# Kernel tuning notes

Measured on AMD Instinct MI355X. Metric: run time of the kernel, lower is better.

## Reference

```python
import jax, jax.numpy as jnp
import numpy as np

L = 9  # local window size


def local_windows(x, l):
    # x: (n, c, h, w) -> (n, c, l*l, h, w): all l*l shifted views (zero-padded),
    # equivalent to F.unfold(x, kernel=(l,l), stride=1, padding=l//2).
    n, c, h, w = x.shape
    pad = l // 2
    xp = jnp.pad(x, ((0, 0), (0, 0), (pad, pad), (pad, pad)))
    views = [xp[:, :, i:i + h, j:j + w] for i in range(l) for j in range(l)]
    return jnp.stack(views, axis=2)


def setup_inputs() -> dict:
    key = jax.random.key(0)
    k1, k2, k3 = jax.random.split(key, 3)
    n, c, h, w = 2, 128, 64, 64
    ft = jax.random.normal(k1, (n, c, h, w), dtype=jnp.float32)
    fk = jax.random.normal(k2, (n, c, h, w), dtype=jnp.float32)
    # 1x1 conv weight shared between key and query projections: (out_c, in_c)
    W = jax.random.normal(k3, (128, 128), dtype=jnp.float32) * (1.0 / np.sqrt(128))
    return {"ft": ft, "fk": fk, "W": W}


def reference(ft, fk, W):
    # 1x1 conv == channel matmul
    key = jnp.einsum('oi,nihw->nohw', W, ft)    # key from frame t
    query = jnp.einsum('oi,nihw->nohw', W, fk)  # query from frame k
    # f_similar(query, key, L): per-pixel query dotted with L*L local keys
    key_win = local_windows(key, L)             # (n, c, L*L, h, w)
    sim = jnp.einsum('nchw,nckhw->nhwk', query, key_win)  # (n, h, w, L*L)
    weight = jax.nn.softmax(sim, axis=-1)
    # f_weighting(ft, weight, L): weighted sum of L*L local raw-ft vectors
    ft_win = local_windows(ft, L)                # (n, c, L*L, h, w)
    out = jnp.einsum('nckhw,nhwk->nchw', ft_win, weight)
    return out
```

## Files before the change

kernel.cpp:

```cpp
#include <hip/hip_runtime.h>
#include <hip/hip_bf16.h>


#define Hh 64
#define Ww 64
#define Cc 128
#define Nn 2
#define KK 81
#define HW (Hh * Ww)
#define CHW (Cc * HW)
#define P_TOT (Nn * HW)

typedef _Float16 h8 __attribute__((ext_vector_type(8)));
typedef _Float16 h4 __attribute__((ext_vector_type(4)));
typedef float f4v __attribute__((ext_vector_type(4)));

#ifndef __has_builtin
#define __has_builtin(x) 0
#endif

#if __has_builtin(__builtin_amdgcn_ds_read_tr16_b64_v4f16)
#define TR_BUILTIN 1
typedef __fp16 g4 __attribute__((__vector_size__(4 * sizeof(__fp16))));
static __device__ __forceinline__ h4 tr16(const _Float16* p) {
    g4 r = __builtin_amdgcn_ds_read_tr16_b64_v4f16(
        (__attribute__((address_space(3))) g4*)p);
    return __builtin_bit_cast(h4, r);
}
#else
#define TR_BUILTIN 0
static __device__ __forceinline__ h4 tr16(const _Float16* p) {
    h4 r;
    asm volatile("ds_read_b64_tr_b16 %0, %1"
                 : "=v"(r)
                 : "v"((__attribute__((address_space(3))) _Float16*)p));
    return r;
}
#endif

__global__ __launch_bounds__(256) void proj_kernel(const float* __restrict__ ft,
                                                   const float* __restrict__ fk,
                                                   const float* __restrict__ Wm,
                                                   _Float16* __restrict__ Qbuf,
                                                   _Float16* __restrict__ Kbuf,
                                                   _Float16* __restrict__ fth) {
    __shared__ __align__(16) _Float16 Wth[128 * 136];
    __shared__ __align__(16) _Float16 xkh[16 * 136];
    __shared__ __align__(16) _Float16 xqh[16 * 136];
    const int t = threadIdx.x;
    const int p0 = blockIdx.x * 16;
    const int nn = p0 >> 12;
    const int gbase = nn * CHW + (p0 & 4095);

#pragma unroll 4
    for (int e = t; e < 4096; e += 256) {
        const int n = e >> 5, ch = e & 31;
        const float4 v = *(const float4*)&Wm[n * 128 + (ch << 2)];
        h4 hv; hv[0] = (_Float16)v.x; hv[1] = (_Float16)v.y;
               hv[2] = (_Float16)v.z; hv[3] = (_Float16)v.w;
        *(h4*)&Wth[n * 136 + (ch << 2)] = hv;
    }
#pragma unroll
    for (int e = t; e < 512; e += 256) {
        const int c = e >> 2, pc = e & 3;
        const float4 vk = *(const float4*)&ft[gbase + c * HW + (pc << 2)];
        const float4 vq = *(const float4*)&fk[gbase + c * HW + (pc << 2)];
        const int px = pc << 2;
        xkh[(px    ) * 136 + c] = (_Float16)vk.x;
        xkh[(px + 1) * 136 + c] = (_Float16)vk.y;
        xkh[(px + 2) * 136 + c] = (_Float16)vk.z;
        xkh[(px + 3) * 136 + c] = (_Float16)vk.w;
        xqh[(px    ) * 136 + c] = (_Float16)vq.x;
        xqh[(px + 1) * 136 + c] = (_Float16)vq.y;
        xqh[(px + 2) * 136 + c] = (_Float16)vq.z;
        xqh[(px + 3) * 136 + c] = (_Float16)vq.w;
    }
    __syncthreads();

    {
        const int px = t >> 4, cq = t & 15;
        *(h8*)&fth[(size_t)(p0 + px) * 128 + (cq << 3)] =
            *(const h8*)&xkh[px * 136 + (cq << 3)];
    }

    const int lane = t & 63, wv = t >> 6;
    const int quad = lane >> 4, l15 = lane & 15;
    const _Float16* xs = (wv >> 1) ? xqh : xkh;
    _Float16* dst = (wv >> 1) ? Qbuf : Kbuf;
    const int nt0 = (wv & 1) << 2;
    const int abase = l15 * 136 + (quad << 3);
    const h8 a0 = *(const h8*)&xs[abase];
    const h8 a1 = *(const h8*)&xs[abase + 32];
    const h8 a2 = *(const h8*)&xs[abase + 64];
    const h8 a3 = *(const h8*)&xs[abase + 96];
#pragma unroll
    for (int ni = 0; ni < 4; ++ni) {
        const int nt = nt0 + ni;
        const int bbase = (nt * 16 + l15) * 136 + (quad << 3);
        const h8 b0 = *(const h8*)&Wth[bbase];
        const h8 b1 = *(const h8*)&Wth[bbase + 32];
        const h8 b2 = *(const h8*)&Wth[bbase + 64];
        const h8 b3 = *(const h8*)&Wth[bbase + 96];
        f4v acc = {0.f, 0.f, 0.f, 0.f};
        acc = __builtin_amdgcn_mfma_f32_16x16x32_f16(a0, b0, acc, 0, 0, 0);
        acc = __builtin_amdgcn_mfma_f32_16x16x32_f16(a1, b1, acc, 0, 0, 0);
        acc = __builtin_amdgcn_mfma_f32_16x16x32_f16(a2, b2, acc, 0, 0, 0);
        acc = __builtin_amdgcn_mfma_f32_16x16x32_f16(a3, b3, acc, 0, 0, 0);
        const int col = nt * 16 + l15;
        const size_t rb = (size_t)(p0 + (quad << 2)) * 128 + col;
#pragma unroll
        for (int r = 0; r < 4; ++r)
            dst[rb + (size_t)r * 128] = (_Float16)acc[r];
    }
}

#define FTL_CH 2312
__global__ __launch_bounds__(256, 4) void sim_weight_kernel(const _Float16* __restrict__ Qbuf,
                                                            const _Float16* __restrict__ Kbuf,
                                                            const _Float16* __restrict__ fth,
                                                            float* __restrict__ out) {
    __shared__ __align__(16) unsigned char smem[40720];
    _Float16* Ksw  = (_Float16*)smem;
    _Float16* Qsw  = (_Float16*)(smem + 36864);
    _Float16* ftl  = (_Float16*)smem;
    _Float16* simb = (_Float16*)(smem + 39168);
    float*    redM = (float*)(smem + 40464);
    float*    redS = (float*)(smem + 40592);

    const int t  = threadIdx.x;
    const int b  = blockIdx.x;
    const int x0 = (b & 7) << 3;
    const int y  = (b >> 3) & 63;
    const int nn = b >> 9;
    const int pg0 = (nn << 12) + (y << 6) + x0;

#pragma unroll 3
    for (int e = t; e < 144 * 16; e += 256) {
        const int v = e >> 4, ci = e & 15;
        const int gx = x0 + (v & 15) - 4;
        const int gy = y + (v >> 4) - 4;
        h8 val = {0, 0, 0, 0, 0, 0, 0, 0};
        if ((unsigned)gx < 64u && (unsigned)gy < 64u)
            val = *(const h8*)&Kbuf[(size_t)((nn << 12) + (gy << 6) + gx) * 128 + (ci << 3)];
        *(h8*)&Ksw[(v << 7) + ((ci ^ (v & 15)) << 3)] = val;
    }
    if (t < 128) {
        const int v = t >> 4, ci = t & 15;
        *(h8*)&Qsw[(v << 7) + ((ci ^ v) << 3)] =
            *(const h8*)&Qbuf[(size_t)(pg0 + v) * 128 + (ci << 3)];
    }
    __syncthreads();

    h8 pf[9];
#pragma unroll
    for (int i = 0; i < 9; ++i) {
        const int e = t + (i << 8);
        const int v = e >> 4, ci = e & 15;
        const int gx = x0 + (v & 15) - 4;
        const int gy = y + (v >> 4) - 4;
        h8 val = {0, 0, 0, 0, 0, 0, 0, 0};
        if ((unsigned)gx < 64u && (unsigned)gy < 64u)
            val = *(const h8*)&fth[(size_t)((nn << 12) + (gy << 6) + gx) * 128 + (ci << 3)];
        pf[i] = val;
    }

    const int lane = t & 63, wv = t >> 6;
    const int quad = lane >> 4, l15 = lane & 15;
    const int qrow = l15 & 7;
    h8 qb[4];
#pragma unroll
    for (int kc = 0; kc < 4; ++kc) {
        const int ci = (kc << 2) + quad;
        qb[kc] = *(const h8*)&Qsw[(qrow << 7) + ((ci ^ qrow) << 3)];
    }
    const int r0 = wv, r1 = wv + 4;
    f4v acc0 = {0.f,0.f,0.f,0.f}, acc1 = acc0, acc2 = acc0;
#pragma unroll
    for (int kc = 0; kc < 4; ++kc) {
        const int ci = (kc << 2) + quad;
        const h8 kA = *(const h8*)&Ksw[(((r0 << 4) + l15) << 7) + ((ci ^ l15) << 3)];
        const h8 kB = *(const h8*)&Ksw[(((r1 << 4) + l15) << 7) + ((ci ^ l15) << 3)];
        const h8 kC = *(const h8*)&Ksw[(((8  << 4) + l15) << 7) + ((ci ^ l15) << 3)];
        acc0 = __builtin_amdgcn_mfma_f32_16x16x32_f16(kA, qb[kc], acc0, 0, 0, 0);
        acc1 = __builtin_amdgcn_mfma_f32_16x16x32_f16(kB, qb[kc], acc1, 0, 0, 0);
        acc2 = __builtin_amdgcn_mfma_f32_16x16x32_f16(kC, qb[kc], acc2, 0, 0, 0);
    }

    float m = -3.0e38f;
#pragma unroll
    for (int reg = 0; reg < 4; ++reg) {
        const int dx = (quad << 2) + reg - l15;
        const bool ok = (l15 < 8) && ((unsigned)dx < 9u);
        if (ok) {
            m = fmaxf(m, fmaxf(acc0[reg], acc1[reg]));
            m = fmaxf(m, acc2[reg]);
        }
    }
    m = fmaxf(m, __shfl_xor(m, 16));
    m = fmaxf(m, __shfl_xor(m, 32));
    if (quad == 0 && l15 < 8) redM[(wv << 3) + l15] = m;
    __syncthreads();

#pragma unroll
    for (int i = 0; i < 9; ++i) {
        const int e = t + (i << 8);
        const int v = e >> 4, ci = e & 15;
        *(h8*)&ftl[(ci >> 1) * FTL_CH + (v << 4) + ((ci & 1) << 3)] = pf[i];
    }

    const float mm = fmaxf(fmaxf(redM[qrow], redM[8 + qrow]),
                           fmaxf(redM[16 + qrow], redM[24 + qrow]));
    float ssum = 0.f;
#pragma unroll
    for (int reg = 0; reg < 4; ++reg) {
        const int dx = (quad << 2) + reg - l15;
        const bool ok = (l15 < 8) && ((unsigned)dx < 9u);
        const float e0 = ok ? __expf(acc0[reg] - mm) : 0.f;
        const float e1 = ok ? __expf(acc1[reg] - mm) : 0.f;
        const float e2 = (ok && wv == 0) ? __expf(acc2[reg] - mm) : 0.f;
        if (ok)            simb[((r0 * 9 + dx) << 3) + l15] = (_Float16)e0;
        if (ok)            simb[((r1 * 9 + dx) << 3) + l15] = (_Float16)e1;
        if (ok && wv == 0) simb[((8  * 9 + dx) << 3) + l15] = (_Float16)e2;
        ssum += e0 + e1 + e2;
    }
    ssum += __shfl_xor(ssum, 16);
    ssum += __shfl_xor(ssum, 32);
    if (quad == 0 && l15 < 8) redS[(wv << 3) + l15] = ssum;
    __syncthreads();

    const _Float16* ftc0 = ftl + wv * FTL_CH;
    const _Float16* ftc1 = ftl + (wv + 4) * FTL_CH;
    h4 bfr[18];
#pragma unroll
    for (int r = 0; r < 9; ++r) {
        bfr[r]     = tr16(ftc0 + (r << 8) + (lane << 2));
        bfr[9 + r] = tr16(ftc1 + (r << 8) + (lane << 2));
    }

#if !TR_BUILTIN
    asm volatile("s_waitcnt lgkmcnt(0)");
    __builtin_amdgcn_sched_barrier(0);
#endif

    f4v aw0 = {0.f, 0.f, 0.f, 0.f}, aw1 = aw0;
#pragma unroll
    for (int r = 0; r < 9; ++r) {
        h4 afr;
#pragma unroll
        for (int j = 0; j < 4; ++j) {
            const int dx = (quad << 2) + j - qrow;
            const bool ok = (unsigned)dx < 9u;
            afr[j] = ok ? simb[(((r * 9 + dx) << 3) + qrow)] : (_Float16)0.f;
        }
        aw0 = __builtin_amdgcn_mfma_f32_16x16x16f16(afr, bfr[r],     aw0, 0, 0, 0);
        aw1 = __builtin_amdgcn_mfma_f32_16x16x16f16(afr, bfr[9 + r], aw1, 0, 0, 0);
    }

    if (quad < 2) {
        const int q4 = quad << 2;
        const float4 rs0 = *(const float4*)&redS[q4];
        const float4 rs1 = *(const float4*)&redS[8 + q4];
        const float4 rs2 = *(const float4*)&redS[16 + q4];
        const float4 rs3 = *(const float4*)&redS[24 + q4];
        const float iv0 = 1.f / (rs0.x + rs1.x + rs2.x + rs3.x);
        const float iv1 = 1.f / (rs0.y + rs1.y + rs2.y + rs3.y);
        const float iv2 = 1.f / (rs0.z + rs1.z + rs2.z + rs3.z);
        const float iv3 = 1.f / (rs0.w + rs1.w + rs2.w + rs3.w);
        const int xb = (y << 6) + x0 + q4;
        const size_t ob0 = ((size_t)((nn << 7) + (wv << 4) + l15) << 12) + xb;
        const size_t ob1 = ((size_t)((nn << 7) + ((wv + 4) << 4) + l15) << 12) + xb;
        float4 o0, o1;
        o0.x = aw0[0] * iv0; o0.y = aw0[1] * iv1; o0.z = aw0[2] * iv2; o0.w = aw0[3] * iv3;
        o1.x = aw1[0] * iv0; o1.y = aw1[1] * iv1; o1.z = aw1[2] * iv2; o1.w = aw1[3] * iv3;
        *(float4*)&out[ob0] = o0;
        *(float4*)&out[ob1] = o1;
    }
}

extern "C" void kernel_launch(void* const* d_in, const int* in_sizes, int n_in,
                              void* d_out, int out_size, void* d_ws, size_t ws_size,
                              hipStream_t stream) {
    const float* ft = (const float*)d_in[0];
    const float* fk = (const float*)d_in[1];
    const float* Wm = (const float*)d_in[2];
    float* out = (float*)d_out;

    _Float16* wsh  = (_Float16*)d_ws;
    _Float16* Qbuf = wsh;
    _Float16* Kbuf = wsh + 1048576;
    _Float16* fth  = wsh + 2097152;

    proj_kernel<<<512, 256, 0, stream>>>(ft, fk, Wm, Qbuf, Kbuf, fth);
    sim_weight_kernel<<<1024, 256, 0, stream>>>(Qbuf, Kbuf, fth, out);
}
```

Measured before the change: 76.79 us.

## Fuse projection into similarity kernel, recomputing key projection per window tile

Merges the 1x1-conv projection kernel and the similarity/weighting kernel into a single kernel. Each block loads the raw fp32 ft halo window (9x16 pixels) and its 8 query pixels from fk, converts them to fp16 in shared memory, and runs the key and query projections with MFMA before the existing softmax and weighting stages. The raw ft tile then serves directly as the weighting operand. This removes the intermediate Q/K/fth global buffers and one launch, at the cost of recomputing the key projection for overlapping halos (about 18x redundant work), reloading W in every block, and doubling shared memory, which lowers occupancy to 2 blocks per CU.

```diff
diff --git a/kernel.cpp b/kernel.cpp
--- a/kernel.cpp
+++ b/kernel.cpp
@@ -9,7 +9,8 @@
 #define KK 81
 #define HW (Hh * Ww)
 #define CHW (Cc * HW)
-#define P_TOT (Nn * HW)
+
+#define FTL_CH 2312
 
 typedef _Float16 h8 __attribute__((ext_vector_type(8)));
 typedef _Float16 h4 __attribute__((ext_vector_type(4)));
@@ -38,135 +39,114 @@
 }
 #endif
 
-__global__ __launch_bounds__(256) void proj_kernel(const float* __restrict__ ft,
-                                                   const float* __restrict__ fk,
-                                                   const float* __restrict__ Wm,
-                                                   _Float16* __restrict__ Qbuf,
-                                                   _Float16* __restrict__ Kbuf,
-                                                   _Float16* __restrict__ fth) {
-    __shared__ __align__(16) _Float16 Wth[128 * 136];
-    __shared__ __align__(16) _Float16 xkh[16 * 136];
-    __shared__ __align__(16) _Float16 xqh[16 * 136];
-    const int t = threadIdx.x;
-    const int p0 = blockIdx.x * 16;
-    const int nn = p0 >> 12;
-    const int gbase = nn * CHW + (p0 & 4095);
-
-#pragma unroll 4
-    for (int e = t; e < 4096; e += 256) {
-        const int n = e >> 5, ch = e & 31;
-        const float4 v = *(const float4*)&Wm[n * 128 + (ch << 2)];
-        h4 hv; hv[0] = (_Float16)v.x; hv[1] = (_Float16)v.y;
-               hv[2] = (_Float16)v.z; hv[3] = (_Float16)v.w;
-        *(h4*)&Wth[n * 136 + (ch << 2)] = hv;
-    }
-#pragma unroll
-    for (int e = t; e < 512; e += 256) {
-        const int c = e >> 2, pc = e & 3;
-        const float4 vk = *(const float4*)&ft[gbase + c * HW + (pc << 2)];
-        const float4 vq = *(const float4*)&fk[gbase + c * HW + (pc << 2)];
-        const int px = pc << 2;
-        xkh[(px    ) * 136 + c] = (_Float16)vk.x;
-        xkh[(px + 1) * 136 + c] = (_Float16)vk.y;
-        xkh[(px + 2) * 136 + c] = (_Float16)vk.z;
-        xkh[(px + 3) * 136 + c] = (_Float16)vk.w;
-        xqh[(px    ) * 136 + c] = (_Float16)vq.x;
-        xqh[(px + 1) * 136 + c] = (_Float16)vq.y;
-        xqh[(px + 2) * 136 + c] = (_Float16)vq.z;
-        xqh[(px + 3) * 136 + c] = (_Float16)vq.w;
-    }
-    __syncthreads();
-
-    {
-        const int px = t >> 4, cq = t & 15;
-        *(h8*)&fth[(size_t)(p0 + px) * 128 + (cq << 3)] =
-            *(const h8*)&xkh[px * 136 + (cq << 3)];
-    }
-
-    const int lane = t & 63, wv = t >> 6;
-    const int quad = lane >> 4, l15 = lane & 15;
-    const _Float16* xs = (wv >> 1) ? xqh : xkh;
-    _Float16* dst = (wv >> 1) ? Qbuf : Kbuf;
-    const int nt0 = (wv & 1) << 2;
-    const int abase = l15 * 136 + (quad << 3);
-    const h8 a0 = *(const h8*)&xs[abase];
-    const h8 a1 = *(const h8*)&xs[abase + 32];
-    const h8 a2 = *(const h8*)&xs[abase + 64];
-    const h8 a3 = *(const h8*)&xs[abase + 96];
-#pragma unroll
-    for (int ni = 0; ni < 4; ++ni) {
-        const int nt = nt0 + ni;
-        const int bbase = (nt * 16 + l15) * 136 + (quad << 3);
-        const h8 b0 = *(const h8*)&Wth[bbase];
-        const h8 b1 = *(const h8*)&Wth[bbase + 32];
-        const h8 b2 = *(const h8*)&Wth[bbase + 64];
-        const h8 b3 = *(const h8*)&Wth[bbase + 96];
-        f4v acc = {0.f, 0.f, 0.f, 0.f};
-        acc = __builtin_amdgcn_mfma_f32_16x16x32_f16(a0, b0, acc, 0, 0, 0);
-        acc = __builtin_amdgcn_mfma_f32_16x16x32_f16(a1, b1, acc, 0, 0, 0);
-        acc = __builtin_amdgcn_mfma_f32_16x16x32_f16(a2, b2, acc, 0, 0, 0);
-        acc = __builtin_amdgcn_mfma_f32_16x16x32_f16(a3, b3, acc, 0, 0, 0);
-        const int col = nt * 16 + l15;
-        const size_t rb = (size_t)(p0 + (quad << 2)) * 128 + col;
-#pragma unroll
-        for (int r = 0; r < 4; ++r)
-            dst[rb + (size_t)r * 128] = (_Float16)acc[r];
-    }
-}
-
-#define FTL_CH 2312
-__global__ __launch_bounds__(256, 4) void sim_weight_kernel(const _Float16* __restrict__ Qbuf,
-                                                            const _Float16* __restrict__ Kbuf,
-                                                            const _Float16* __restrict__ fth,
-                                                            float* __restrict__ out) {
-    __shared__ __align__(16) unsigned char smem[40720];
-    _Float16* Ksw  = (_Float16*)smem;
-    _Float16* Qsw  = (_Float16*)(smem + 36864);
-    _Float16* ftl  = (_Float16*)smem;
-    _Float16* simb = (_Float16*)(smem + 39168);
-    float*    redM = (float*)(smem + 40464);
-    float*    redS = (float*)(smem + 40592);
+__global__ __launch_bounds__(256, 2) void ila_fused(const float* __restrict__ ft,
+                                                    const float* __restrict__ fk,
+                                                    const float* __restrict__ Wm,
+                                                    float* __restrict__ out) {
+    __shared__ __align__(16) unsigned char smem[79632];
+    _Float16* xw   = (_Float16*)(smem);
+    _Float16* Wth  = (_Float16*)(smem + 36992);
+    _Float16* Ksw  = (_Float16*)(smem + 36992);
+    _Float16* Qsw  = (_Float16*)(smem + 73856);
+    _Float16* simb = (_Float16*)(smem + 75904);
+    float*    redM = (float*)(smem + 77200);
+    float*    redS = (float*)(smem + 77328);
+    _Float16* xq   = (_Float16*)(smem + 77456);
 
     const int t  = threadIdx.x;
     const int b  = blockIdx.x;
     const int x0 = (b & 7) << 3;
     const int y  = (b >> 3) & 63;
     const int nn = b >> 9;
-    const int pg0 = (nn << 12) + (y << 6) + x0;
-
-#pragma unroll 3
-    for (int e = t; e < 144 * 16; e += 256) {
-        const int v = e >> 4, ci = e & 15;
-        const int gx = x0 + (v & 15) - 4;
-        const int gy = y + (v >> 4) - 4;
-        h8 val = {0, 0, 0, 0, 0, 0, 0, 0};
-        if ((unsigned)gx < 64u && (unsigned)gy < 64u)
-            val = *(const h8*)&Kbuf[(size_t)((nn << 12) + (gy << 6) + gx) * 128 + (ci << 3)];
-        *(h8*)&Ksw[(v << 7) + ((ci ^ (v & 15)) << 3)] = val;
-    }
-    if (t < 128) {
-        const int v = t >> 4, ci = t & 15;
-        *(h8*)&Qsw[(v << 7) + ((ci ^ v) << 3)] =
-            *(const h8*)&Qbuf[(size_t)(pg0 + v) * 128 + (ci << 3)];
-    }
-    __syncthreads();
-
-    h8 pf[9];
-#pragma unroll
-    for (int i = 0; i < 9; ++i) {
+
+#pragma unroll 4
+    for (int e = t; e < 4096; e += 256) {
+        const int o = e >> 5, ch = e & 31;
+        const float4 v = *(const float4*)&Wm[o * 128 + (ch << 2)];
+        h4 hv; hv[0] = (_Float16)v.x; hv[1] = (_Float16)v.y;
+               hv[2] = (_Float16)v.z; hv[3] = (_Float16)v.w;
+        *(h4*)&Wth[o * 136 + (ch << 2)] = hv;
+    }
+
+#pragma unroll
+    for (int i = 0; i < 18; ++i) {
         const int e = t + (i << 8);
-        const int v = e >> 4, ci = e & 15;
-        const int gx = x0 + (v & 15) - 4;
-        const int gy = y + (v >> 4) - 4;
-        h8 val = {0, 0, 0, 0, 0, 0, 0, 0};
-        if ((unsigned)gx < 64u && (unsigned)gy < 64u)
-            val = *(const h8*)&fth[(size_t)((nn << 12) + (gy << 6) + gx) * 128 + (ci << 3)];
-        pf[i] = val;
-    }
+        const int xb = e & 3, c = (e >> 2) & 127, r = e >> 9;
+        const int gx0 = x0 + (xb << 2) - 4;
+        const int gy  = y + r - 4;
+        float4 v = make_float4(0.f, 0.f, 0.f, 0.f);
+        if ((unsigned)gx0 <= 60u && (unsigned)gy < 64u)
+            v = *(const float4*)&ft[nn * CHW + c * HW + (gy << 6) + gx0];
+        _Float16* base = &xw[(c >> 4) * FTL_CH + (r << 8) + (xb << 6) + (c & 15)];
+        base[0]  = (_Float16)v.x;
+        base[16] = (_Float16)v.y;
+        base[32] = (_Float16)v.z;
+        base[48] = (_Float16)v.w;
+    }
+
+    {
+        const int xb = t & 1, c = t >> 1;
+        const float4 v = *(const float4*)&fk[nn * CHW + c * HW + (y << 6) + x0 + (xb << 2)];
+        _Float16* base = &xq[((xb << 2)) * 136 + c];
+        base[0]   = (_Float16)v.x;
+        base[136] = (_Float16)v.y;
+        base[272] = (_Float16)v.z;
+        base[408] = (_Float16)v.w;
+    }
+    __syncthreads();
 
     const int lane = t & 63, wv = t >> 6;
     const int quad = lane >> 4, l15 = lane & 15;
     const int qrow = l15 & 7;
+
+    f4v accK[9][2];
+    f4v accQ[2];
+#pragma unroll
+    for (int pt = 0; pt < 9; ++pt) {
+        accK[pt][0] = (f4v){0.f, 0.f, 0.f, 0.f};
+        accK[pt][1] = (f4v){0.f, 0.f, 0.f, 0.f};
+    }
+    accQ[0] = (f4v){0.f, 0.f, 0.f, 0.f};
+    accQ[1] = (f4v){0.f, 0.f, 0.f, 0.f};
+#pragma unroll
+    for (int kc = 0; kc < 4; ++kc) {
+        const int c0 = (kc << 5) + (quad << 3);
+        const h8 bw0 = *(const h8*)&Wth[((wv << 5) + l15) * 136 + c0];
+        const h8 bw1 = *(const h8*)&Wth[((wv << 5) + 16 + l15) * 136 + c0];
+        const h8 aq  = *(const h8*)&xq[qrow * 136 + c0];
+        accQ[0] = __builtin_amdgcn_mfma_f32_16x16x32_f16(bw0, aq, accQ[0], 0, 0, 0);
+        accQ[1] = __builtin_amdgcn_mfma_f32_16x16x32_f16(bw1, aq, accQ[1], 0, 0, 0);
+        const int xoff = ((c0 >> 4) * FTL_CH) + (c0 & 15);
+#pragma unroll
+        for (int pt = 0; pt < 9; ++pt) {
+            const h8 ax = *(const h8*)&xw[xoff + (pt << 8) + (l15 << 4)];
+            accK[pt][0] = __builtin_amdgcn_mfma_f32_16x16x32_f16(bw0, ax, accK[pt][0], 0, 0, 0);
+            accK[pt][1] = __builtin_amdgcn_mfma_f32_16x16x32_f16(bw1, ax, accK[pt][1], 0, 0, 0);
+        }
+    }
+    __syncthreads();
+
+    {
+        const int q4 = (quad & 1) << 2;
+#pragma unroll
+        for (int ni = 0; ni < 2; ++ni) {
+            const int ci = ((wv << 1) + ni) * 2 + (quad >> 1);
+#pragma unroll
+            for (int pt = 0; pt < 9; ++pt) {
+                const int v = (pt << 4) + l15;
+                h4 hk; hk[0] = (_Float16)accK[pt][ni][0]; hk[1] = (_Float16)accK[pt][ni][1];
+                       hk[2] = (_Float16)accK[pt][ni][2]; hk[3] = (_Float16)accK[pt][ni][3];
+                *(h4*)&Ksw[(v << 7) + ((ci ^ l15) << 3) + q4] = hk;
+            }
+            if (l15 < 8) {
+                h4 hq; hq[0] = (_Float16)accQ[ni][0]; hq[1] = (_Float16)accQ[ni][1];
+                       hq[2] = (_Float16)accQ[ni][2]; hq[3] = (_Float16)accQ[ni][3];
+                *(h4*)&Qsw[(l15 << 7) + ((ci ^ l15) << 3) + q4] = hq;
+            }
+        }
+    }
+    __syncthreads();
+
     h8 qb[4];
 #pragma unroll
     for (int kc = 0; kc < 4; ++kc) {
@@ -174,7 +154,7 @@
         qb[kc] = *(const h8*)&Qsw[(qrow << 7) + ((ci ^ qrow) << 3)];
     }
     const int r0 = wv, r1 = wv + 4;
-    f4v acc0 = {0.f,0.f,0.f,0.f}, acc1 = acc0, acc2 = acc0;
+    f4v acc0 = {0.f, 0.f, 0.f, 0.f}, acc1 = acc0, acc2 = acc0;
 #pragma unroll
     for (int kc = 0; kc < 4; ++kc) {
         const int ci = (kc << 2) + quad;
@@ -201,11 +181,13 @@
     if (quad == 0 && l15 < 8) redM[(wv << 3) + l15] = m;
     __syncthreads();
 
-#pragma unroll
-    for (int i = 0; i < 9; ++i) {
-        const int e = t + (i << 8);
-        const int v = e >> 4, ci = e & 15;
-        *(h8*)&ftl[(ci >> 1) * FTL_CH + (v << 4) + ((ci & 1) << 3)] = pf[i];
+    const _Float16* ftc0 = xw + wv * FTL_CH;
+    const _Float16* ftc1 = xw + (wv + 4) * FTL_CH;
+    h4 bfr[18];
+#pragma unroll
+    for (int r = 0; r < 9; ++r) {
+        bfr[r]     = tr16(ftc0 + (r << 8) + (lane << 2));
+        bfr[9 + r] = tr16(ftc1 + (r << 8) + (lane << 2));
     }
 
     const float mm = fmaxf(fmaxf(redM[qrow], redM[8 + qrow]),
@@ -227,15 +209,6 @@
     ssum += __shfl_xor(ssum, 32);
     if (quad == 0 && l15 < 8) redS[(wv << 3) + l15] = ssum;
     __syncthreads();
-
-    const _Float16* ftc0 = ftl + wv * FTL_CH;
-    const _Float16* ftc1 = ftl + (wv + 4) * FTL_CH;
-    h4 bfr[18];
-#pragma unroll
-    for (int r = 0; r < 9; ++r) {
-        bfr[r]     = tr16(ftc0 + (r << 8) + (lane << 2));
-        bfr[9 + r] = tr16(ftc1 + (r << 8) + (lane << 2));
-    }
 
 #if !TR_BUILTIN
     asm volatile("s_waitcnt lgkmcnt(0)");
@@ -284,12 +257,7 @@
     const float* fk = (const float*)d_in[1];
     const float* Wm = (const float*)d_in[2];
     float* out = (float*)d_out;
-
-    _Float16* wsh  = (_Float16*)d_ws;
-    _Float16* Qbuf = wsh;
-    _Float16* Kbuf = wsh + 1048576;
-    _Float16* fth  = wsh + 2097152;
-
-    proj_kernel<<<512, 256, 0, stream>>>(ft, fk, Wm, Qbuf, Kbuf, fth);
-    sim_weight_kernel<<<1024, 256, 0, stream>>>(Qbuf, Kbuf, fth, out);
-}
+    (void)d_ws; (void)ws_size;
+
+    ila_fused<<<1024, 256, 0, stream>>>(ft, fk, Wm, out);
+}
```

After: 84.30 us. 9.8% more time.

## Process two output rows per block to fill MFMA tiles and reuse halos

Applied to the files above, without the earlier changes.

Each block of the similarity/weighting kernel now covers an 8x2 pixel tile instead of 8x1. The 16 query pixels fill the full MFMA N dimension, which removes the padded half-empty tiles, and the key and ft halo loads (10 rows instead of 9) are shared across two output rows. Queries are read straight from global memory instead of being staged in LDS. The grid halves to 512 blocks and launch bounds drop to 3 waves per SIMD, so there is less parallelism and more register and LDS pressure per block.

```diff
diff --git a/kernel.cpp b/kernel.cpp
--- a/kernel.cpp
+++ b/kernel.cpp
@@ -6,10 +6,8 @@
 #define Ww 64
 #define Cc 128
 #define Nn 2
-#define KK 81
 #define HW (Hh * Ww)
 #define CHW (Cc * HW)
-#define P_TOT (Nn * HW)
 
 typedef _Float16 h8 __attribute__((ext_vector_type(8)));
 typedef _Float16 h4 __attribute__((ext_vector_type(4)));
@@ -114,50 +112,44 @@
     }
 }
 
-#define FTL_CH 2312
-__global__ __launch_bounds__(256, 4) void sim_weight_kernel(const _Float16* __restrict__ Qbuf,
+#define FTL2 2568
+__global__ __launch_bounds__(256, 3) void sim_weight_kernel(const _Float16* __restrict__ Qbuf,
                                                             const _Float16* __restrict__ Kbuf,
                                                             const _Float16* __restrict__ fth,
                                                             float* __restrict__ out) {
-    __shared__ __align__(16) unsigned char smem[40720];
+    __shared__ __align__(16) unsigned char smem[44192];
     _Float16* Ksw  = (_Float16*)smem;
-    _Float16* Qsw  = (_Float16*)(smem + 36864);
     _Float16* ftl  = (_Float16*)smem;
-    _Float16* simb = (_Float16*)(smem + 39168);
-    float*    redM = (float*)(smem + 40464);
-    float*    redS = (float*)(smem + 40592);
+    _Float16* simb = (_Float16*)(smem + 41088);
+    float*    redM = (float*)(smem + 43680);
+    float*    redS = (float*)(smem + 43936);
 
     const int t  = threadIdx.x;
     const int b  = blockIdx.x;
     const int x0 = (b & 7) << 3;
-    const int y  = (b >> 3) & 63;
-    const int nn = b >> 9;
-    const int pg0 = (nn << 12) + (y << 6) + x0;
-
-#pragma unroll 3
-    for (int e = t; e < 144 * 16; e += 256) {
+    const int y0 = ((b >> 3) & 31) << 1;
+    const int nn = b >> 8;
+
+#pragma unroll
+    for (int i = 0; i < 10; ++i) {
+        const int e = t + (i << 8);
         const int v = e >> 4, ci = e & 15;
         const int gx = x0 + (v & 15) - 4;
-        const int gy = y + (v >> 4) - 4;
+        const int gy = y0 + (v >> 4) - 4;
         h8 val = {0, 0, 0, 0, 0, 0, 0, 0};
         if ((unsigned)gx < 64u && (unsigned)gy < 64u)
             val = *(const h8*)&Kbuf[(size_t)((nn << 12) + (gy << 6) + gx) * 128 + (ci << 3)];
         *(h8*)&Ksw[(v << 7) + ((ci ^ (v & 15)) << 3)] = val;
     }
-    if (t < 128) {
-        const int v = t >> 4, ci = t & 15;
-        *(h8*)&Qsw[(v << 7) + ((ci ^ v) << 3)] =
-            *(const h8*)&Qbuf[(size_t)(pg0 + v) * 128 + (ci << 3)];
-    }
     __syncthreads();
 
-    h8 pf[9];
-#pragma unroll
-    for (int i = 0; i < 9; ++i) {
+    h8 pf[10];
+#pragma unroll
+    for (int i = 0; i < 10; ++i) {
         const int e = t + (i << 8);
         const int v = e >> 4, ci = e & 15;
         const int gx = x0 + (v & 15) - 4;
-        const int gy = y + (v >> 4) - 4;
+        const int gy = y0 + (v >> 4) - 4;
         h8 val = {0, 0, 0, 0, 0, 0, 0, 0};
         if ((unsigned)gx < 64u && (unsigned)gy < 64u)
             val = *(const h8*)&fth[(size_t)((nn << 12) + (gy << 6) + gx) * 128 + (ci << 3)];
@@ -166,75 +158,92 @@
 
     const int lane = t & 63, wv = t >> 6;
     const int quad = lane >> 4, l15 = lane & 15;
-    const int qrow = l15 & 7;
-    h8 qb[4];
+    const int py = l15 >> 3, px = l15 & 7;
+    const size_t pgQ = (size_t)((nn << 12) + ((y0 + py) << 6) + x0 + px) * 128;
+    f4v sa = {0.f, 0.f, 0.f, 0.f}, sb = sa, sc = sa, sd = sa;
 #pragma unroll
     for (int kc = 0; kc < 4; ++kc) {
         const int ci = (kc << 2) + quad;
-        qb[kc] = *(const h8*)&Qsw[(qrow << 7) + ((ci ^ qrow) << 3)];
-    }
-    const int r0 = wv, r1 = wv + 4;
-    f4v acc0 = {0.f,0.f,0.f,0.f}, acc1 = acc0, acc2 = acc0;
-#pragma unroll
-    for (int kc = 0; kc < 4; ++kc) {
-        const int ci = (kc << 2) + quad;
-        const h8 kA = *(const h8*)&Ksw[(((r0 << 4) + l15) << 7) + ((ci ^ l15) << 3)];
-        const h8 kB = *(const h8*)&Ksw[(((r1 << 4) + l15) << 7) + ((ci ^ l15) << 3)];
-        const h8 kC = *(const h8*)&Ksw[(((8  << 4) + l15) << 7) + ((ci ^ l15) << 3)];
-        acc0 = __builtin_amdgcn_mfma_f32_16x16x32_f16(kA, qb[kc], acc0, 0, 0, 0);
-        acc1 = __builtin_amdgcn_mfma_f32_16x16x32_f16(kB, qb[kc], acc1, 0, 0, 0);
-        acc2 = __builtin_amdgcn_mfma_f32_16x16x32_f16(kC, qb[kc], acc2, 0, 0, 0);
+        const h8 q  = *(const h8*)&Qbuf[pgQ + (ci << 3)];
+        const h8 kA = *(const h8*)&Ksw[((((wv    ) << 4) + l15) << 7) + ((ci ^ l15) << 3)];
+        const h8 kB = *(const h8*)&Ksw[((((wv + 4) << 4) + l15) << 7) + ((ci ^ l15) << 3)];
+        const h8 kC = *(const h8*)&Ksw[((((8     ) << 4) + l15) << 7) + ((ci ^ l15) << 3)];
+        const h8 kD = *(const h8*)&Ksw[((((9     ) << 4) + l15) << 7) + ((ci ^ l15) << 3)];
+        sa = __builtin_amdgcn_mfma_f32_16x16x32_f16(kA, q, sa, 0, 0, 0);
+        sb = __builtin_amdgcn_mfma_f32_16x16x32_f16(kB, q, sb, 0, 0, 0);
+        sc = __builtin_amdgcn_mfma_f32_16x16x32_f16(kC, q, sc, 0, 0, 0);
+        sd = __builtin_amdgcn_mfma_f32_16x16x32_f16(kD, q, sd, 0, 0, 0);
     }
 
     float m = -3.0e38f;
 #pragma unroll
     for (int reg = 0; reg < 4; ++reg) {
-        const int dx = (quad << 2) + reg - l15;
-        const bool ok = (l15 < 8) && ((unsigned)dx < 9u);
-        if (ok) {
-            m = fmaxf(m, fmaxf(acc0[reg], acc1[reg]));
-            m = fmaxf(m, acc2[reg]);
+        const int dx = (quad << 2) + reg - px;
+        if ((unsigned)dx < 9u) {
+            if ((unsigned)(wv - py) < 9u) m = fmaxf(m, sa[reg]);
+            m = fmaxf(m, sb[reg]);
+            m = fmaxf(m, sc[reg]);
+            if (py) m = fmaxf(m, sd[reg]);
         }
     }
     m = fmaxf(m, __shfl_xor(m, 16));
     m = fmaxf(m, __shfl_xor(m, 32));
-    if (quad == 0 && l15 < 8) redM[(wv << 3) + l15] = m;
+    if (quad == 0) redM[(wv << 4) + l15] = m;
     __syncthreads();
 
 #pragma unroll
-    for (int i = 0; i < 9; ++i) {
+    for (int i = 0; i < 10; ++i) {
         const int e = t + (i << 8);
         const int v = e >> 4, ci = e & 15;
-        *(h8*)&ftl[(ci >> 1) * FTL_CH + (v << 4) + ((ci & 1) << 3)] = pf[i];
-    }
-
-    const float mm = fmaxf(fmaxf(redM[qrow], redM[8 + qrow]),
-                           fmaxf(redM[16 + qrow], redM[24 + qrow]));
+        *(h8*)&ftl[(ci >> 1) * FTL2 + (v << 4) + ((ci & 1) << 3)] = pf[i];
+    }
+
+    const float mm = fmaxf(fmaxf(redM[l15], redM[16 + l15]),
+                           fmaxf(redM[32 + l15], redM[48 + l15]));
     float ssum = 0.f;
 #pragma unroll
     for (int reg = 0; reg < 4; ++reg) {
-        const int dx = (quad << 2) + reg - l15;
-        const bool ok = (l15 < 8) && ((unsigned)dx < 9u);
-        const float e0 = ok ? __expf(acc0[reg] - mm) : 0.f;
-        const float e1 = ok ? __expf(acc1[reg] - mm) : 0.f;
-        const float e2 = (ok && wv == 0) ? __expf(acc2[reg] - mm) : 0.f;
-        if (ok)            simb[((r0 * 9 + dx) << 3) + l15] = (_Float16)e0;
-        if (ok)            simb[((r1 * 9 + dx) << 3) + l15] = (_Float16)e1;
-        if (ok && wv == 0) simb[((8  * 9 + dx) << 3) + l15] = (_Float16)e2;
-        ssum += e0 + e1 + e2;
+        const int dx = (quad << 2) + reg - px;
+        const bool okx = (unsigned)dx < 9u;
+        {
+            const int ry = wv - py;
+            const bool ok = okx && ((unsigned)ry < 9u);
+            const float e = ok ? __expf(sa[reg] - mm) : 0.f;
+            if (ok) simb[((ry * 9 + dx) << 4) + l15] = (_Float16)e;
+            ssum += e;
+        }
+        {
+            const int ry = wv + 4 - py;
+            const float e = okx ? __expf(sb[reg] - mm) : 0.f;
+            if (okx) simb[((ry * 9 + dx) << 4) + l15] = (_Float16)e;
+            ssum += e;
+        }
+        {
+            const int ry = 8 - py;
+            const bool ok = okx && (wv == 0);
+            const float e = ok ? __expf(sc[reg] - mm) : 0.f;
+            if (ok) simb[((ry * 9 + dx) << 4) + l15] = (_Float16)e;
+            ssum += e;
+        }
+        {
+            const bool ok = okx && (wv == 1) && (py == 1);
+            const float e = ok ? __expf(sd[reg] - mm) : 0.f;
+            if (ok) simb[((8 * 9 + dx) << 4) + l15] = (_Float16)e;
+            ssum += e;
+        }
     }
     ssum += __shfl_xor(ssum, 16);
     ssum += __shfl_xor(ssum, 32);
-    if (quad == 0 && l15 < 8) redS[(wv << 3) + l15] = ssum;
+    if (quad == 0) redS[(wv << 4) + l15] = ssum;
     __syncthreads();
 
-    const _Float16* ftc0 = ftl + wv * FTL_CH;
-    const _Float16* ftc1 = ftl + (wv + 4) * FTL_CH;
-    h4 bfr[18];
-#pragma unroll
-    for (int r = 0; r < 9; ++r) {
-        bfr[r]     = tr16(ftc0 + (r << 8) + (lane << 2));
-        bfr[9 + r] = tr16(ftc1 + (r << 8) + (lane << 2));
+    const _Float16* ftc0 = ftl + wv * FTL2;
+    const _Float16* ftc1 = ftl + (wv + 4) * FTL2;
+    h4 bfr[20];
+#pragma unroll
+    for (int r = 0; r < 10; ++r) {
+        bfr[r]      = tr16(ftc0 + (r << 8) + (lane << 2));
+        bfr[10 + r] = tr16(ftc1 + (r << 8) + (lane << 2));
     }
 
 #if !TR_BUILTIN
@@ -244,31 +253,32 @@
 
     f4v aw0 = {0.f, 0.f, 0.f, 0.f}, aw1 = aw0;
 #pragma unroll
-    for (int r = 0; r < 9; ++r) {
+    for (int r = 0; r < 10; ++r) {
+        const int ry = r - py;
+        const bool okr = (unsigned)ry < 9u;
         h4 afr;
 #pragma unroll
         for (int j = 0; j < 4; ++j) {
-            const int dx = (quad << 2) + j - qrow;
-            const bool ok = (unsigned)dx < 9u;
-            afr[j] = ok ? simb[(((r * 9 + dx) << 3) + qrow)] : (_Float16)0.f;
-        }
-        aw0 = __builtin_amdgcn_mfma_f32_16x16x16f16(afr, bfr[r],     aw0, 0, 0, 0);
-        aw1 = __builtin_amdgcn_mfma_f32_16x16x16f16(afr, bfr[9 + r], aw1, 0, 0, 0);
-    }
-
-    if (quad < 2) {
-        const int q4 = quad << 2;
-        const float4 rs0 = *(const float4*)&redS[q4];
-        const float4 rs1 = *(const float4*)&redS[8 + q4];
-        const float4 rs2 = *(const float4*)&redS[16 + q4];
-        const float4 rs3 = *(const float4*)&redS[24 + q4];
-        const float iv0 = 1.f / (rs0.x + rs1.x + rs2.x + rs3.x);
-        const float iv1 = 1.f / (rs0.y + rs1.y + rs2.y + rs3.y);
-        const float iv2 = 1.f / (rs0.z + rs1.z + rs2.z + rs3.z);
-        const float iv3 = 1.f / (rs0.w + rs1.w + rs2.w + rs3.w);
-        const int xb = (y << 6) + x0 + q4;
-        const size_t ob0 = ((size_t)((nn << 7) + (wv << 4) + l15) << 12) + xb;
-        const size_t ob1 = ((size_t)((nn << 7) + ((wv + 4) << 4) + l15) << 12) + xb;
+            const int dx = (quad << 2) + j - px;
+            const bool ok = okr && ((unsigned)dx < 9u);
+            afr[j] = ok ? simb[(((ry * 9 + dx) << 4)) + l15] : (_Float16)0.f;
+        }
+        aw0 = __builtin_amdgcn_mfma_f32_16x16x16f16(afr, bfr[r],      aw0, 0, 0, 0);
+        aw1 = __builtin_amdgcn_mfma_f32_16x16x16f16(afr, bfr[10 + r], aw1, 0, 0, 0);
+    }
+
+    {
+        const int p0q = quad << 2;
+        const float iv0 = 1.f / (redS[p0q    ] + redS[16 + p0q    ] + redS[32 + p0q    ] + redS[48 + p0q    ]);
+        const float iv1 = 1.f / (redS[p0q + 1] + redS[16 + p0q + 1] + redS[32 + p0q + 1] + redS[48 + p0q + 1]);
+        const float iv2 = 1.f / (redS[p0q + 2] + redS[16 + p0q + 2] + redS[32 + p0q + 2] + redS[48 + p0q + 2]);
+        const float iv3 = 1.f / (redS[p0q + 3] + redS[16 + p0q + 3] + redS[32 + p0q + 3] + redS[48 + p0q + 3]);
+        const int yo = y0 + (p0q >> 3);
+        const int xb = (yo << 6) + x0 + (p0q & 7);
+        const int c0 = (wv << 4) + l15;
+        const int c1 = ((wv + 4) << 4) + l15;
+        const size_t ob0 = ((size_t)((nn << 7) + c0) << 12) + xb;
+        const size_t ob1 = ((size_t)((nn << 7) + c1) << 12) + xb;
         float4 o0, o1;
         o0.x = aw0[0] * iv0; o0.y = aw0[1] * iv1; o0.z = aw0[2] * iv2; o0.w = aw0[3] * iv3;
         o1.x = aw1[0] * iv0; o1.y = aw1[1] * iv1; o1.z = aw1[2] * iv2; o1.w = aw1[3] * iv3;
@@ -291,5 +301,5 @@
     _Float16* fth  = wsh + 2097152;
 
     proj_kernel<<<512, 256, 0, stream>>>(ft, fk, Wm, Qbuf, Kbuf, fth);
-    sim_weight_kernel<<<1024, 256, 0, stream>>>(Qbuf, Kbuf, fth, out);
-}
+    sim_weight_kernel<<<512, 256, 0, stream>>>(Qbuf, Kbuf, fth, out);
+}
```

Measured after the change: 76.93 us (median of 2 runs). About the same (+0.2%).
